# Performance work log

Measured on AMD Instinct MI355X. Metric: run time of the kernel, lower is better.

## Reference

```python
import jax, jax.numpy as jnp
import numpy as np

B, T, H, W, C = 8, 16, 64, 64, 16
HID = 64  # hidden_dim of each ConvLSTM cell
K = 3     # kernel size


def _convlstm_step(x, h, c, Wk, b):
    # conv over concat([x, h]) -> 4*HID gate channels (i, f, o, g)
    z = jax.lax.conv_general_dilated(
        jnp.concatenate([x, h], axis=-1), Wk,
        window_strides=(1, 1), padding='SAME',
        dimension_numbers=('NHWC', 'HWIO', 'NHWC')) + b
    i, f, o, g = jnp.split(z, 4, axis=-1)
    c_new = jax.nn.sigmoid(f) * c + jax.nn.sigmoid(i) * jnp.tanh(g)
    h_new = jax.nn.sigmoid(o) * jnp.tanh(c_new)
    return h_new, c_new


def setup_inputs() -> dict:
    key = jax.random.key(0)
    k1, k2, k3 = jax.random.split(key, 3)
    enc_input = jax.random.normal(k1, (B, T, H, W, C), jnp.float32)
    # input cell: in_channels = C + HID; stacked hidden cell: 2*HID
    W0 = jax.random.normal(k2, (K, K, C + HID, 4 * HID), jnp.float32) * 0.05
    b0 = jnp.zeros((4 * HID,), jnp.float32)
    W1 = jax.random.normal(k3, (K, K, 2 * HID, 4 * HID), jnp.float32) * 0.05
    b1 = jnp.zeros((4 * HID,), jnp.float32)
    return {"enc_input": enc_input, "W0": W0, "b0": b0, "W1": W1, "b1": b1}


def reference(enc_input, W0, b0, W1, b1):
    Bv, Tv, Hv, Wv, _ = enc_input.shape
    z0 = jnp.zeros((Bv, Hv, Wv, HID), enc_input.dtype)

    def step(carry, x_t):
        h0, c0, h1, c1 = carry
        h0, c0 = _convlstm_step(x_t, h0, c0, W0, b0)   # input ConvLSTM
        h1, c1 = _convlstm_step(h0, h1, c1, W1, b1)    # stacked hidden ConvLSTM
        return (h0, c0, h1, c1), None

    xs = jnp.moveaxis(enc_input, 1, 0)  # [T, B, H, W, C]
    (h0, c0, h1, c1), _ = jax.lax.scan(step, (z0, z0, z0, z0), xs)
    # Encoder returns last hidden layer's (h, c)
    return (h1, c1)
```

## Files before the change

kernel.cpp:

```cpp
#include <hip/hip_runtime.h>
#include <hip/hip_bf16.h>

#define Bv 8
#define Tv 16
#define Hv 64
#define Wv 64
#define Cv 16
#define HID 64
#define PH 66

typedef short short8 __attribute__((ext_vector_type(8)));
typedef float f32x4 __attribute__((ext_vector_type(4)));
typedef unsigned short u16x8 __attribute__((ext_vector_type(8)));

__device__ __forceinline__ unsigned short f2bf(float x) {
  union { float f; unsigned int u; } v; v.f = x;
  unsigned int r = v.u + 0x7FFF + ((v.u >> 16) & 1);
  return (unsigned short)(r >> 16);
}
__device__ __forceinline__ float sigmoid_f(float x) {
  return 1.f / (1.f + __expf(-x));
}
__device__ __forceinline__ float tanh_f(float x) {
  float e = __expf(2.f * x);
  return 1.f - 2.f / (e + 1.f);
}

__global__ void relayout_w0(const float* __restrict__ W0, unsigned short* __restrict__ out) {
  int o = blockIdx.x * 256 + threadIdx.x;
  if (o >= 27 * 8192) return;
  int cc = o >> 13, t = o & 8191;
  int wn = t >> 11, t2 = t & 2047;
  int g = t2 >> 9, t3 = t2 & 511;
  int l = t3 >> 3, e = t3 & 7;
  int kg = l >> 4, r = l & 15;
  int k = kg * 8 + e;
  int col = g * 64 + wn * 16 + r;
  int tap = cc / 3, cgi = cc - tap * 3;
  int p = cgi * 32 + k;
  float v = 0.f;
  if (p < 16)        v = W0[(size_t)(tap * 80 + p) * 256 + col];
  else if (p >= 32)  v = W0[(size_t)(tap * 80 + (p - 16)) * 256 + col];
  out[o] = f2bf(v);
}
__global__ void relayout_w1(const float* __restrict__ W1, unsigned short* __restrict__ out) {
  int o = blockIdx.x * 256 + threadIdx.x;
  if (o >= 36 * 8192) return;
  int cc = o >> 13, t = o & 8191;
  int wn = t >> 11, t2 = t & 2047;
  int g = t2 >> 9, t3 = t2 & 511;
  int l = t3 >> 3, e = t3 & 7;
  int kg = l >> 4, r = l & 15;
  int k = kg * 8 + e;
  int col = g * 64 + wn * 16 + r;
  int tap = cc >> 2, cgi = cc & 3;
  out[o] = f2bf(W1[(size_t)(tap * 128 + cgi * 32 + k) * 256 + col]);
}

__global__ void convert_x0(const float* __restrict__ enc, unsigned short* __restrict__ xb) {
  int idx = blockIdx.x * 256 + threadIdx.x;
  int b = idx >> 12, pix = idx & 4095;
  int y = pix >> 6, x = pix & 63;
  const float* s = enc + ((size_t)(b * Tv + 0) * 4096 + pix) * 16;
  float4 f0 = *(const float4*)(s);
  float4 f1 = *(const float4*)(s + 4);
  float4 f2 = *(const float4*)(s + 8);
  float4 f3 = *(const float4*)(s + 12);
  u16x8 o0, o1;
  o0[0]=f2bf(f0.x); o0[1]=f2bf(f0.y); o0[2]=f2bf(f0.z); o0[3]=f2bf(f0.w);
  o0[4]=f2bf(f1.x); o0[5]=f2bf(f1.y); o0[6]=f2bf(f1.z); o0[7]=f2bf(f1.w);
  o1[0]=f2bf(f2.x); o1[1]=f2bf(f2.y); o1[2]=f2bf(f2.z); o1[3]=f2bf(f2.w);
  o1[4]=f2bf(f3.x); o1[5]=f2bf(f3.y); o1[6]=f2bf(f3.z); o1[7]=f2bf(f3.w);
  unsigned short* d = xb + ((size_t)((b * PH + y + 1) * PH) + (x + 1)) * 32;
  *(u16x8*)(d)     = o0;
  *(u16x8*)(d + 8) = o1;
}

template<int CELL>
__global__ __launch_bounds__(512, 2)
void cell_mfma(const unsigned short* __restrict__ A0, const unsigned short* __restrict__ A1,
               const unsigned short* __restrict__ Wr, const float* __restrict__ bias,
               float* __restrict__ cbuf, unsigned short* __restrict__ hout,
               float* __restrict__ h1f, float* __restrict__ c1f,
               const float* __restrict__ enc, int tnext, unsigned short* __restrict__ xnext)
{
  constexpr int CG = (CELL == 0) ? 3 : 4;
  constexpr int NC = 9 * CG;
  extern __shared__ char lds[];

  const int tid = threadIdx.x;
  const int l = tid & 63, w = tid >> 6;
  const int wm = w >> 2, wn = w & 3;
  const int gid = blockIdx.x;
  const int bx = gid & 7, by = (gid >> 3) & 3, b = gid >> 5;
  const int r = l & 15, kg = l >> 4;
  const int j = wn * 16 + r;

  const char* bases[2] = {(const char*)A0, (const char*)A1};

  unsigned offsA[CG];
  {
    int ps = w * 16 + r;
    int ys = by * 16 + (ps >> 3), xs = bx * 8 + (ps & 7);
    int pixs = (b * PH + ys) * PH + xs;
#pragma unroll
    for (int cgi = 0; cgi < CG; ++cgi) {
      int chb = (CELL == 0) ? (cgi == 0 ? 64 : 128) : 128;
      int cho = (CELL == 0) ? (cgi == 2 ? 64 : 0) : ((cgi & 1) * 64);
      offsA[cgi] = (unsigned)(pixs * chb + cho + kg * 16);
    }
  }

  float bi[4];
#pragma unroll
  for (int g = 0; g < 4; ++g) bi[g] = bias[g * 64 + j];
  float cpre[4][4];
#pragma unroll
  for (int mi = 0; mi < 4; ++mi) {
#pragma unroll
    for (int rg = 0; rg < 4; ++rg) {
      int p = wm * 64 + mi * 16 + kg * 4 + rg;
      int y = by * 16 + (p >> 3), x = bx * 8 + (p & 7);
      cpre[mi][rg] = cbuf[((size_t)((b * Hv + y) * Wv) + x) * HID + j];
    }
  }
  asm volatile("s_waitcnt vmcnt(0)" ::: "memory");
  __builtin_amdgcn_sched_barrier(0);

  auto ISSUE = [&](int cc, int buf) {
    char* dst = lds + buf * 24576;
    int tap, cgi;
    if (CELL == 0) { tap = cc / 3; cgi = cc - tap * 3; }
    else           { tap = cc >> 2; cgi = cc & 3; }
    int ky = tap / 3, kx = tap - ky * 3;
    const char* srcb;
    unsigned toff;
    if (CELL == 0) {
      if (cgi == 0) { srcb = bases[0]; toff = (unsigned)((ky * PH + kx) * 64); }
      else          { srcb = bases[1]; toff = (unsigned)((ky * PH + kx) * 128); }
    } else {
      srcb = bases[cgi >> 1];
      toff = (unsigned)((ky * PH + kx) * 128);
    }
    __builtin_amdgcn_global_load_lds((const unsigned int*)(srcb + offsA[cgi] + toff),
                                     (unsigned int*)(dst + w * 1024), 16, 0, 0);
    const char* wp = (const char*)Wr + (size_t)cc * 16384 + (unsigned)(w * 2048 + l * 16);
    __builtin_amdgcn_global_load_lds((const unsigned int*)(wp),
                                     (unsigned int*)(dst + 8192 + w * 2048), 16, 0, 0);
    __builtin_amdgcn_global_load_lds((const unsigned int*)(wp + 1024),
                                     (unsigned int*)(dst + 8192 + w * 2048 + 1024), 16, 0, 0);
  };

  f32x4 acc[4][4] = {};
  short8 af[2][4], bfv[2][4];

  ISSUE(0, 0); ISSUE(1, 1); ISSUE(2, 2);
#pragma unroll
  for (int cc = 0; cc < NC; ++cc) {
    if (cc <= NC - 3)      { asm volatile("s_waitcnt vmcnt(6)" ::: "memory"); }
    else if (cc == NC - 2) { asm volatile("s_waitcnt vmcnt(3)" ::: "memory"); }
    else                   { asm volatile("s_waitcnt vmcnt(0)" ::: "memory"); }
    __builtin_amdgcn_sched_barrier(0);
    __builtin_amdgcn_s_barrier();
    __builtin_amdgcn_sched_barrier(0);

    const int q = cc & 1;
    const char* bufp = lds + (cc % 5) * 24576;
#pragma unroll
    for (int mi = 0; mi < 4; ++mi)
      af[q][mi] = *(const short8*)(bufp + (wm * 4 + mi) * 1024 + l * 16);
#pragma unroll
    for (int g = 0; g < 4; ++g)
      bfv[q][g] = *(const short8*)(bufp + 8192 + (wn * 4 + g) * 1024 + l * 16);

    if (cc + 3 < NC) ISSUE(cc + 3, (cc + 3) % 5);

    if (cc > 0) {
      asm volatile("s_waitcnt lgkmcnt(8)" ::: "memory");
      __builtin_amdgcn_sched_barrier(0);
      const int qp = q ^ 1;
#pragma unroll
      for (int mi = 0; mi < 4; ++mi)
#pragma unroll
        for (int g = 0; g < 4; ++g)
          acc[mi][g] = __builtin_amdgcn_mfma_f32_16x16x32_bf16(
              af[qp][mi], bfv[qp][g], acc[mi][g], 0, 0, 0);
    }
  }
  asm volatile("s_waitcnt lgkmcnt(0)" ::: "memory");
  __builtin_amdgcn_sched_barrier(0);
  {
    const int qp = (NC - 1) & 1;
#pragma unroll
    for (int mi = 0; mi < 4; ++mi)
#pragma unroll
      for (int g = 0; g < 4; ++g)
        acc[mi][g] = __builtin_amdgcn_mfma_f32_16x16x32_bf16(
            af[qp][mi], bfv[qp][g], acc[mi][g], 0, 0, 0);
  }

#pragma unroll
  for (int mi = 0; mi < 4; ++mi) {
#pragma unroll
    for (int rg = 0; rg < 4; ++rg) {
      int p = wm * 64 + mi * 16 + kg * 4 + rg;
      int y = by * 16 + (p >> 3), x = bx * 8 + (p & 7);
      float zi = acc[mi][0][rg] + bi[0];
      float zf = acc[mi][1][rg] + bi[1];
      float zo = acc[mi][2][rg] + bi[2];
      float zg = acc[mi][3][rg] + bi[3];
      float co = cpre[mi][rg];
      float cn = sigmoid_f(zf) * co + sigmoid_f(zi) * tanh_f(zg);
      float hn = sigmoid_f(zo) * tanh_f(cn);
      size_t ci = ((size_t)((b * Hv + y) * Wv) + x) * HID + j;
      cbuf[ci] = cn;
      hout[((size_t)((b * PH + y + 1) * PH) + (x + 1)) * HID + j] = f2bf(hn);
      if (CELL == 1 && h1f != nullptr) {
        h1f[ci] = hn;
        c1f[ci] = cn;
      }
    }
  }

  if (CELL == 1 && tnext < Tv) {
    int px = gid * 128 + (tid >> 2), q4 = tid & 3;
    int bb = px >> 12, pix = px & 4095;
    int y = pix >> 6, x = pix & 63;
    const float* s = enc + ((size_t)(bb * Tv + tnext) * 4096 + pix) * 16 + q4 * 4;
    float4 f = *(const float4*)s;
    unsigned short* d = xnext + ((size_t)((bb * PH + y + 1) * PH) + (x + 1)) * 32 + q4 * 4;
    d[0] = f2bf(f.x); d[1] = f2bf(f.y); d[2] = f2bf(f.z); d[3] = f2bf(f.w);
  }
}

extern "C" void kernel_launch(void* const* d_in, const int* in_sizes, int n_in,
                              void* d_out, int out_size, void* d_ws, size_t ws_size,
                              hipStream_t stream) {
  const float* enc = (const float*)d_in[0];
  const float* W0  = (const float*)d_in[1];
  const float* b0  = (const float*)d_in[2];
  const float* W1  = (const float*)d_in[3];
  const float* b1  = (const float*)d_in[4];

  float* out = (float*)d_out;
  const size_t NST = (size_t)Bv * Hv * Wv * HID;
  float* h1f = out;
  float* c1  = out + NST;

  char* ws = (char*)d_ws;
  const size_t SZ_C = NST * 4;
  const size_t SZ_H = (size_t)Bv * PH * PH * HID * 2;
  const size_t SZ_X = (size_t)Bv * PH * PH * 32 * 2;
  float*          c0  = (float*)ws;
  unsigned short* h0a = (unsigned short*)(ws + SZ_C);
  unsigned short* h0b = (unsigned short*)(ws + SZ_C + SZ_H);
  unsigned short* h1a = (unsigned short*)(ws + SZ_C + 2 * SZ_H);
  unsigned short* h1b = (unsigned short*)(ws + SZ_C + 3 * SZ_H);
  unsigned short* xb  = (unsigned short*)(ws + SZ_C + 4 * SZ_H);
  unsigned short* w0r = (unsigned short*)(ws + SZ_C + 4 * SZ_H + SZ_X);
  unsigned short* w1r = (unsigned short*)(ws + SZ_C + 4 * SZ_H + SZ_X + (size_t)27 * 16384);

  hipFuncSetAttribute((const void*)cell_mfma<0>, hipFuncAttributeMaxDynamicSharedMemorySize, 131072);
  hipFuncSetAttribute((const void*)cell_mfma<1>, hipFuncAttributeMaxDynamicSharedMemorySize, 131072);

  hipMemsetAsync(ws, 0, SZ_C + 4 * SZ_H + SZ_X, stream);
  hipMemsetAsync(c1, 0, SZ_C, stream);

  relayout_w0<<<864, 256, 0, stream>>>(W0, w0r);
  relayout_w1<<<1152, 256, 0, stream>>>(W1, w1r);
  convert_x0<<<128, 256, 0, stream>>>(enc, xb);

  dim3 grid(256), block(512);
  for (int t = 0; t < Tv; ++t) {
    const bool last = (t == Tv - 1);
    unsigned short* h0r = (t & 1) ? h0b : h0a;
    unsigned short* h0w = (t & 1) ? h0a : h0b;
    unsigned short* h1r = (t & 1) ? h1b : h1a;
    unsigned short* h1w = (t & 1) ? h1a : h1b;
    cell_mfma<0><<<grid, block, 122880, stream>>>(
        xb, h0r, w0r, b0, c0, h0w, nullptr, nullptr, nullptr, Tv, nullptr);
    cell_mfma<1><<<grid, block, 122880, stream>>>(
        h0w, h1r, w1r, b1, c1, h1w, last ? h1f : nullptr, last ? c1 : nullptr,
        enc, t + 1, xb);
  }
}
```

Measured before the change: 725.1 us.

## Specialize first timestep to skip zero-state convolution and deepen load prefetch

Adds a T0 template variant used at t=0 that skips the hidden-state channel groups (known zero) and the cell-state loads, cutting the conv K dimension for the first step of each cell. It replaces the full workspace memsets with a kernel that zeroes only the padded borders of the h buffers plus the x buffer. It also deepens the global-to-LDS prefetch from 3 to 4 chunks in flight and moves the issue point after the LDS fragment wait. The deeper prefetch reuses the 5-slot ring with less slack, so the barrier ordering matters. Correctness depends on the interior of the h buffers always being written before it is read.

```diff
diff --git a/kernel.cpp b/kernel.cpp
--- a/kernel.cpp
+++ b/kernel.cpp
@@ -55,6 +55,27 @@
   int col = g * 64 + wn * 16 + r;
   int tap = cc >> 2, cgi = cc & 3;
   out[o] = f2bf(W1[(size_t)(tap * 128 + cgi * 32 + k) * 256 + col]);
+}
+
+__global__ void zero_init(unsigned short* __restrict__ h0a, unsigned short* __restrict__ h0b,
+                          unsigned short* __restrict__ h1a, unsigned short* __restrict__ h1b,
+                          unsigned short* __restrict__ xb) {
+  int idx = blockIdx.x * 256 + threadIdx.x;
+  u16x8 z = {};
+  const int XB_CH = (Bv * PH * PH * 32 * 2) / 16;
+  if (idx < XB_CH) { *(u16x8*)(xb + idx * 8) = z; return; }
+  idx -= XB_CH;
+  int bufi = idx / 16640;
+  if (bufi >= 4) return;
+  int rem = idx - bufi * 16640;
+  int b = rem / 2080, r2 = rem - b * 2080;
+  int hp = r2 >> 3, c8 = r2 & 7;
+  int y, x;
+  if (hp < 66)       { y = 0;  x = hp; }
+  else if (hp < 132) { y = 65; x = hp - 66; }
+  else { int i2 = hp - 132; y = 1 + (i2 >> 1); x = (i2 & 1) * 65; }
+  unsigned short* base = (bufi == 0) ? h0a : (bufi == 1) ? h0b : (bufi == 2) ? h1a : h1b;
+  *(u16x8*)(base + ((size_t)((b * PH + y) * PH) + x) * 64 + c8 * 8) = z;
 }
 
 __global__ void convert_x0(const float* __restrict__ enc, unsigned short* __restrict__ xb) {
@@ -76,7 +97,7 @@
   *(u16x8*)(d + 8) = o1;
 }
 
-template<int CELL>
+template<int CELL, bool T0>
 __global__ __launch_bounds__(512, 2)
 void cell_mfma(const unsigned short* __restrict__ A0, const unsigned short* __restrict__ A1,
                const unsigned short* __restrict__ Wr, const float* __restrict__ bias,
@@ -84,8 +105,7 @@
                float* __restrict__ h1f, float* __restrict__ c1f,
                const float* __restrict__ enc, int tnext, unsigned short* __restrict__ xnext)
 {
-  constexpr int CG = (CELL == 0) ? 3 : 4;
-  constexpr int NC = 9 * CG;
+  constexpr int NC = T0 ? (CELL == 0 ? 9 : 18) : (CELL == 0 ? 27 : 36);
   extern __shared__ char lds[];
 
   const int tid = threadIdx.x;
@@ -98,53 +118,53 @@
 
   const char* bases[2] = {(const char*)A0, (const char*)A1};
 
-  unsigned offsA[CG];
+  int pixs;
   {
     int ps = w * 16 + r;
     int ys = by * 16 + (ps >> 3), xs = bx * 8 + (ps & 7);
-    int pixs = (b * PH + ys) * PH + xs;
-#pragma unroll
-    for (int cgi = 0; cgi < CG; ++cgi) {
-      int chb = (CELL == 0) ? (cgi == 0 ? 64 : 128) : 128;
-      int cho = (CELL == 0) ? (cgi == 2 ? 64 : 0) : ((cgi & 1) * 64);
-      offsA[cgi] = (unsigned)(pixs * chb + cho + kg * 16);
-    }
+    pixs = (b * PH + ys) * PH + xs;
   }
 
   float bi[4];
 #pragma unroll
   for (int g = 0; g < 4; ++g) bi[g] = bias[g * 64 + j];
-  float cpre[4][4];
-#pragma unroll
-  for (int mi = 0; mi < 4; ++mi) {
-#pragma unroll
-    for (int rg = 0; rg < 4; ++rg) {
-      int p = wm * 64 + mi * 16 + kg * 4 + rg;
-      int y = by * 16 + (p >> 3), x = bx * 8 + (p & 7);
-      cpre[mi][rg] = cbuf[((size_t)((b * Hv + y) * Wv) + x) * HID + j];
-    }
-  }
-  asm volatile("s_waitcnt vmcnt(0)" ::: "memory");
-  __builtin_amdgcn_sched_barrier(0);
+  float cpre[4][4] = {};
+  if constexpr (!T0) {
+#pragma unroll
+    for (int mi = 0; mi < 4; ++mi) {
+#pragma unroll
+      for (int rg = 0; rg < 4; ++rg) {
+        int p = wm * 64 + mi * 16 + kg * 4 + rg;
+        int y = by * 16 + (p >> 3), x = bx * 8 + (p & 7);
+        cpre[mi][rg] = cbuf[((size_t)((b * Hv + y) * Wv) + x) * HID + j];
+      }
+    }
+  }
 
   auto ISSUE = [&](int cc, int buf) {
     char* dst = lds + buf * 24576;
-    int tap, cgi;
-    if (CELL == 0) { tap = cc / 3; cgi = cc - tap * 3; }
-    else           { tap = cc >> 2; cgi = cc & 3; }
+    int tap, cgi, wcc;
+    if (CELL == 0) {
+      if (T0) { tap = cc; cgi = 0; wcc = cc * 3; }
+      else    { tap = cc / 3; cgi = cc - tap * 3; wcc = cc; }
+    } else {
+      if (T0) { tap = cc >> 1; cgi = cc & 1; wcc = tap * 4 + cgi; }
+      else    { tap = cc >> 2; cgi = cc & 3; wcc = cc; }
+    }
     int ky = tap / 3, kx = tap - ky * 3;
     const char* srcb;
-    unsigned toff;
+    unsigned aoff;
     if (CELL == 0) {
-      if (cgi == 0) { srcb = bases[0]; toff = (unsigned)((ky * PH + kx) * 64); }
-      else          { srcb = bases[1]; toff = (unsigned)((ky * PH + kx) * 128); }
+      if (cgi == 0) { srcb = bases[0]; aoff = (unsigned)((pixs + ky * PH + kx) * 64 + kg * 16); }
+      else { srcb = bases[1];
+             aoff = (unsigned)((pixs + ky * PH + kx) * 128 + ((cgi == 2) ? 64 : 0) + kg * 16); }
     } else {
       srcb = bases[cgi >> 1];
-      toff = (unsigned)((ky * PH + kx) * 128);
-    }
-    __builtin_amdgcn_global_load_lds((const unsigned int*)(srcb + offsA[cgi] + toff),
+      aoff = (unsigned)((pixs + ky * PH + kx) * 128 + (cgi & 1) * 64 + kg * 16);
+    }
+    __builtin_amdgcn_global_load_lds((const unsigned int*)(srcb + aoff),
                                      (unsigned int*)(dst + w * 1024), 16, 0, 0);
-    const char* wp = (const char*)Wr + (size_t)cc * 16384 + (unsigned)(w * 2048 + l * 16);
+    const char* wp = (const char*)Wr + (size_t)wcc * 16384 + (unsigned)(w * 2048 + l * 16);
     __builtin_amdgcn_global_load_lds((const unsigned int*)(wp),
                                      (unsigned int*)(dst + 8192 + w * 2048), 16, 0, 0);
     __builtin_amdgcn_global_load_lds((const unsigned int*)(wp + 1024),
@@ -154,10 +174,11 @@
   f32x4 acc[4][4] = {};
   short8 af[2][4], bfv[2][4];
 
-  ISSUE(0, 0); ISSUE(1, 1); ISSUE(2, 2);
+  ISSUE(0, 0); ISSUE(1, 1); ISSUE(2, 2); ISSUE(3, 3);
 #pragma unroll
   for (int cc = 0; cc < NC; ++cc) {
-    if (cc <= NC - 3)      { asm volatile("s_waitcnt vmcnt(6)" ::: "memory"); }
+    if (cc <= NC - 4)      { asm volatile("s_waitcnt vmcnt(9)" ::: "memory"); }
+    else if (cc == NC - 3) { asm volatile("s_waitcnt vmcnt(6)" ::: "memory"); }
     else if (cc == NC - 2) { asm volatile("s_waitcnt vmcnt(3)" ::: "memory"); }
     else                   { asm volatile("s_waitcnt vmcnt(0)" ::: "memory"); }
     __builtin_amdgcn_sched_barrier(0);
@@ -173,11 +194,12 @@
     for (int g = 0; g < 4; ++g)
       bfv[q][g] = *(const short8*)(bufp + 8192 + (wn * 4 + g) * 1024 + l * 16);
 
-    if (cc + 3 < NC) ISSUE(cc + 3, (cc + 3) % 5);
-
     if (cc > 0) {
       asm volatile("s_waitcnt lgkmcnt(8)" ::: "memory");
       __builtin_amdgcn_sched_barrier(0);
+    }
+    if (cc + 4 < NC) ISSUE(cc + 4, (cc + 4) % 5);
+    if (cc > 0) {
       const int qp = q ^ 1;
 #pragma unroll
       for (int mi = 0; mi < 4; ++mi)
@@ -260,12 +282,12 @@
   unsigned short* w0r = (unsigned short*)(ws + SZ_C + 4 * SZ_H + SZ_X);
   unsigned short* w1r = (unsigned short*)(ws + SZ_C + 4 * SZ_H + SZ_X + (size_t)27 * 16384);
 
-  hipFuncSetAttribute((const void*)cell_mfma<0>, hipFuncAttributeMaxDynamicSharedMemorySize, 131072);
-  hipFuncSetAttribute((const void*)cell_mfma<1>, hipFuncAttributeMaxDynamicSharedMemorySize, 131072);
-
-  hipMemsetAsync(ws, 0, SZ_C + 4 * SZ_H + SZ_X, stream);
-  hipMemsetAsync(c1, 0, SZ_C, stream);
-
+  hipFuncSetAttribute((const void*)cell_mfma<0,false>, hipFuncAttributeMaxDynamicSharedMemorySize, 131072);
+  hipFuncSetAttribute((const void*)cell_mfma<0,true>,  hipFuncAttributeMaxDynamicSharedMemorySize, 131072);
+  hipFuncSetAttribute((const void*)cell_mfma<1,false>, hipFuncAttributeMaxDynamicSharedMemorySize, 131072);
+  hipFuncSetAttribute((const void*)cell_mfma<1,true>,  hipFuncAttributeMaxDynamicSharedMemorySize, 131072);
+
+  zero_init<<<805, 256, 0, stream>>>(h0a, h0b, h1a, h1b, xb);
   relayout_w0<<<864, 256, 0, stream>>>(W0, w0r);
   relayout_w1<<<1152, 256, 0, stream>>>(W1, w1r);
   convert_x0<<<128, 256, 0, stream>>>(enc, xb);
@@ -277,10 +299,17 @@
     unsigned short* h0w = (t & 1) ? h0a : h0b;
     unsigned short* h1r = (t & 1) ? h1b : h1a;
     unsigned short* h1w = (t & 1) ? h1a : h1b;
-    cell_mfma<0><<<grid, block, 122880, stream>>>(
-        xb, h0r, w0r, b0, c0, h0w, nullptr, nullptr, nullptr, Tv, nullptr);
-    cell_mfma<1><<<grid, block, 122880, stream>>>(
-        h0w, h1r, w1r, b1, c1, h1w, last ? h1f : nullptr, last ? c1 : nullptr,
-        enc, t + 1, xb);
-  }
-}
+    if (t == 0) {
+      cell_mfma<0,true><<<grid, block, 122880, stream>>>(
+          xb, h0r, w0r, b0, c0, h0w, nullptr, nullptr, nullptr, Tv, nullptr);
+      cell_mfma<1,true><<<grid, block, 122880, stream>>>(
+          h0w, h1r, w1r, b1, c1, h1w, nullptr, nullptr, enc, 1, xb);
+    } else {
+      cell_mfma<0,false><<<grid, block, 122880, stream>>>(
+          xb, h0r, w0r, b0, c0, h0w, nullptr, nullptr, nullptr, Tv, nullptr);
+      cell_mfma<1,false><<<grid, block, 122880, stream>>>(
+          h0w, h1r, w1r, b1, c1, h1w, last ? h1f : nullptr, last ? c1 : nullptr,
+          enc, t + 1, xb);
+    }
+  }
+}
```

Result: no change. 714.8 us (-1.4%).
